# Optimization experiments

Hardware: AMD Instinct MI355X
Metric: run time of the kernel (lower is better)

Reference implementation:

```python
import jax, jax.numpy as jnp
import numpy as np

# graph sizes
G, P, EP = 128, 256, 1024          # graphs, nodes/graph, edges/graph
N, E = G * P, G * EP
C, KENS, S = 4, 2, 1               # centroids, ensembles, samples
R = S * KENS                       # repeats
F, DE, D, OUT = 64, 16, 128, 10


def setup_inputs() -> dict:
    key = jax.random.key(0)
    ks = jax.random.split(key, 24)
    off = (jnp.arange(G, dtype=jnp.int32) * P)[:, None]
    src = (jax.random.randint(ks[0], (G, EP), 0, P, dtype=jnp.int32) + off).reshape(-1)
    dst = (jax.random.randint(ks[1], (G, EP), 0, P, dtype=jnp.int32) + off).reshape(-1)
    edge_index = jnp.stack([src, dst])            # [2, E], edges stay within graphs
    batch = jnp.repeat(jnp.arange(G, dtype=jnp.int32), P)  # [N]
    rn = lambda k, shp, s: jax.random.normal(k, shp, jnp.float32) * s
    return {
        "x_feat": rn(ks[2], (N, F), 1.0),
        "edge_attr": rn(ks[3], (E, DE), 1.0),
        "W_atom": rn(ks[4], (F, D), 0.1), "b_atom": jnp.zeros((D,), jnp.float32),
        "W_score": rn(ks[5], (D, C * KENS), 0.1),
        "W_edge": rn(ks[6], (DE, D), 0.1),
        "W_b2c": rn(ks[7], (D, D), 0.1),
        "W_bb": rn(ks[8], (D, D), 0.1), "W_bc": rn(ks[9], (D, D), 0.1),
        "W_cb": rn(ks[10], (D, D), 0.1), "W_cc": rn(ks[11], (D, D), 0.1),
        "W_sb": rn(ks[12], (D, D), 0.1), "W_sc": rn(ks[13], (D, D), 0.1),
        "W_inter": rn(ks[14], (D, D), 0.1), "b_inter": jnp.zeros((D,), jnp.float32),
        "W_out": rn(ks[15], (D, OUT), 0.1), "b_out": jnp.zeros((OUT,), jnp.float32),
        "edge_index": edge_index, "batch": batch,
    }


def reference(x_feat, edge_attr, W_atom, b_atom, W_score, W_edge, W_b2c,
              W_bb, W_bc, W_cb, W_cc, W_sb, W_sc, W_inter, b_inter,
              W_out, b_out, edge_index, batch):
    src, dst = edge_index[0], edge_index[1]
    # atom encoder + scorer + softmax sampler (marginals)
    x = x_feat @ W_atom + b_atom                                  # [N,D]
    scores = (x @ W_score).reshape(N, C, KENS)
    marg = jax.nn.softmax(scores, axis=1)                         # over centroids
    nm = jnp.broadcast_to(marg[None], (S, N, C, KENS))            # [S,N,C,KENS]
    nm = jnp.transpose(nm, (0, 3, 2, 1)).reshape(R, C, N)         # [R,C,N]
    em = nm[:, :, src] * nm[:, :, dst]                            # edge_mask [R,C,E]
    # base2centroid: masked MP on base graph + weighted segment-mean pooling
    edge_emb = edge_attr @ W_edge                                 # [E,D]
    h = jax.nn.relu(x @ W_b2c)                                    # [N,D]
    m = h[src] + edge_emb                                         # [E,D]
    agg = jnp.zeros((R, C, N, D), m.dtype).at[:, :, dst].add(em[..., None] * m)
    hm = h[None, None] + agg                                      # [R,C,N,D]
    denom = jnp.zeros((R, C, G), nm.dtype).at[:, :, batch].add(nm)
    num = jnp.zeros((R, C, G, D), hm.dtype).at[:, :, batch].add(nm[..., None] * hm)
    cent_x = jnp.transpose(num / (denom[..., None] + 1e-6), (0, 2, 1, 3))  # [R,G,C,D]
    # intra centroid-pair edge weights: triu pairs + diag, scatter over graphs
    iu, ju = np.triu_indices(C, 1)
    pi = np.concatenate([iu, np.arange(C)])
    pj = np.concatenate([ju, np.arange(C)])
    e2g = batch[src]
    w = jnp.zeros((R, pi.size, G), nm.dtype).at[:, :, e2g].add(
        nm[:, pi][:, :, src] * nm[:, pj][:, :, dst])              # [R,10,G]
    w = w.at[:, -C:, :].multiply(0.5)                             # halve diagonal counts
    wt = jnp.transpose(w, (0, 2, 1))                              # [R,G,10]
    Wcc = jnp.zeros((R, G, C, C), nm.dtype)
    Wcc = Wcc.at[:, :, pi, pj].add(wt).at[:, :, pj, pi].add(wt)   # to_undirected
    dg = jnp.arange(C)
    Wcc = Wcc.at[:, :, dg, dg].multiply(0.5)                      # self loops counted once
    Wcc = Wcc / (jax.lax.stop_gradient(jnp.max(Wcc)) + 1e-9)      # detached-max norm
    # hetero GNN layer: base->base, base->centroid, centroid->centroid, centroid->base
    agg_bb = jnp.zeros((N, D), x.dtype).at[dst].add(x[src] + edge_emb)           # [N,D]
    agg_bc = jnp.transpose(
        jnp.zeros((R, C, G, D), x.dtype).at[:, :, batch].add(nm[..., None] * x[None, None]),
        (0, 2, 1, 3))                                             # [R,G,C,D]
    agg_cc = jnp.einsum('rgij,rgjd->rgid', Wcc, cent_x)
    h_cent = jax.nn.relu(agg_bc @ W_bc + agg_cc @ W_cc + cent_x @ W_sc)          # [R,G,C,D]
    agg_cb = jnp.einsum('rcn,rncd->rnd', nm, h_cent[:, batch])                   # [R,N,D]
    h_base = jax.nn.relu(agg_bb[None] @ W_bb + agg_cb @ W_cb + x[None] @ W_sb)   # [R,N,D]
    # inter-ensemble mean pool, inter head, intra mean graph pool, intra head
    node_emb = jnp.mean(h_base, axis=0) @ W_inter + b_inter                      # [N,D]
    graph_emb = jnp.zeros((G, D), node_emb.dtype).at[batch].add(node_emb) / P    # [G,D]
    return graph_emb @ W_out + b_out                                             # [G,OUT]
```

## Files before the change

kernel.cpp:

```cpp
#include <hip/hip_runtime.h>
#include <hip/hip_bf16.h>

#define Nn 32768
#define Ee 131072
#define Gg 128
#define Dd 128

using bf16 = __hip_bfloat16;
typedef __attribute__((ext_vector_type(8))) short bf16x8;
typedef __attribute__((ext_vector_type(4))) float f32x4;

__device__ __forceinline__ float b2f(bf16 v){ return __bfloat162float(v); }
__device__ __forceinline__ bf16  f2b(float v){ return __float2bfloat16(v); }
__device__ __forceinline__ unsigned short bf16bits(float v){
  union { bf16 b; unsigned short u; } cv; cv.b = f2b(v); return cv.u;
}
__device__ __forceinline__ unsigned int packxh(float xv, float hv){
  return ((unsigned int)bf16bits(hv) << 16) | (unsigned int)bf16bits(xv);
}
__device__ __forceinline__ float upk_x(unsigned int v){ return __uint_as_float(v << 16); }
__device__ __forceinline__ float upk_h(unsigned int v){ return __uint_as_float(v & 0xffff0000u); }

__global__ __launch_bounds__(128)
void k_wrep(const float* __restrict__ Wbb, const float* __restrict__ Wsb,
            const float* __restrict__ Wcb, unsigned short* __restrict__ Wbbp,
            unsigned short* __restrict__ Wsbp, unsigned short* __restrict__ Wcbp) {
  int mat = blockIdx.x >> 7, n = blockIdx.x & 127, k = threadIdx.x;
  const float* src = (mat == 0) ? Wbb : (mat == 1) ? Wsb : Wcb;
  unsigned short* dst = (mat == 0) ? Wbbp : (mat == 1) ? Wsbp : Wcbp;
  dst[n*128 + k] = bf16bits(src[k*128 + n]);
}

__global__ __launch_bounds__(256)
void k_atom(const float* __restrict__ xf, const float* __restrict__ Wa,
            const float* __restrict__ ba, const float* __restrict__ Wsc,
            const float* __restrict__ Wb2c,
            unsigned int* __restrict__ xh, float* __restrict__ nmt) {
  __shared__ float sxf[32*64];
  __shared__ float sx[32*128];
  __shared__ float ss[32*8];
  int tid = threadIdx.x, n0 = blockIdx.x * 32;
  int ct = tid & 31, rt = tid >> 5;
  int c0 = ct*4, r0 = rt*4;
  for (int j = tid; j < 2048; j += 256) sxf[j] = xf[n0*64 + j];
  __syncthreads();
  float acc[4][4];
  #pragma unroll
  for (int i = 0; i < 4; ++i)
    #pragma unroll
    for (int j = 0; j < 4; ++j) acc[i][j] = ba[c0+j];
  for (int k = 0; k < 64; ++k) {
    float4 bv = *reinterpret_cast<const float4*>(&Wa[k*128 + c0]);
    #pragma unroll
    for (int i = 0; i < 4; ++i) {
      float a = sxf[(r0+i)*64 + k];
      acc[i][0] += a*bv.x; acc[i][1] += a*bv.y; acc[i][2] += a*bv.z; acc[i][3] += a*bv.w;
    }
  }
  #pragma unroll
  for (int i = 0; i < 4; ++i)
    #pragma unroll
    for (int j = 0; j < 4; ++j) sx[(r0+i)*128 + c0+j] = acc[i][j];
  __syncthreads();
  {
    int node = tid >> 3, col = tid & 7;
    float s = 0.f;
    for (int d = 0; d < 128; ++d) s += sx[node*128 + d] * Wsc[d*8 + col];
    ss[node*8 + col] = s;
  }
  __syncthreads();
  if (tid < 64) {
    int node = tid >> 1, k = tid & 1;
    float v0 = ss[node*8 + 0 + k], v1 = ss[node*8 + 2 + k];
    float v2 = ss[node*8 + 4 + k], v3 = ss[node*8 + 6 + k];
    float mx = fmaxf(fmaxf(v0, v1), fmaxf(v2, v3));
    float e0 = expf(v0-mx), e1 = expf(v1-mx), e2 = expf(v2-mx), e3 = expf(v3-mx);
    float inv = 1.f / (e0+e1+e2+e3);
    size_t nb = (size_t)(n0 + node)*8 + k*4;
    nmt[nb+0] = e0*inv; nmt[nb+1] = e1*inv; nmt[nb+2] = e2*inv; nmt[nb+3] = e3*inv;
  }
  float acc2[4][4];
  #pragma unroll
  for (int i = 0; i < 4; ++i)
    #pragma unroll
    for (int j = 0; j < 4; ++j) acc2[i][j] = 0.f;
  for (int k = 0; k < 128; ++k) {
    float4 bv = *reinterpret_cast<const float4*>(&Wb2c[k*128 + c0]);
    #pragma unroll
    for (int i = 0; i < 4; ++i) {
      float a = sx[(r0+i)*128 + k];
      acc2[i][0] += a*bv.x; acc2[i][1] += a*bv.y; acc2[i][2] += a*bv.z; acc2[i][3] += a*bv.w;
    }
  }
  #pragma unroll
  for (int i = 0; i < 4; ++i)
    #pragma unroll
    for (int j = 0; j < 4; ++j)
      xh[(size_t)(n0+r0+i)*128 + c0+j] = packxh(acc[i][j], fmaxf(acc2[i][j], 0.f));
}

__global__ __launch_bounds__(256)
void k_csr(const int* __restrict__ ei, const float* __restrict__ nmt,
           int* __restrict__ order, int* __restrict__ osrc,
           int* __restrict__ rowstart, float* __restrict__ den) {
  __shared__ int cnt[256], off[256], sdl[1024];
  __shared__ float sden[256*8];
  int t = threadIdx.x, g = blockIdx.x;
  cnt[t] = 0;
  __syncthreads();
  #pragma unroll
  for (int j = 0; j < 4; ++j) {
    int e = t + j*256;
    int dl = ei[Ee + g*1024 + e] - g*256;
    sdl[e] = dl;
    atomicAdd(&cnt[dl], 1);
  }
  {
    const float4* p = reinterpret_cast<const float4*>(nmt + (size_t)(g*256 + t)*8);
    float4 a = p[0], b = p[1];
    sden[t*8+0]=a.x; sden[t*8+1]=a.y; sden[t*8+2]=a.z; sden[t*8+3]=a.w;
    sden[t*8+4]=b.x; sden[t*8+5]=b.y; sden[t*8+6]=b.z; sden[t*8+7]=b.w;
  }
  __syncthreads();
  off[t] = cnt[t];
  __syncthreads();
  for (int s = 1; s < 256; s <<= 1) {
    int v = (t >= s) ? off[t - s] : 0;
    __syncthreads();
    off[t] += v;
    __syncthreads();
  }
  int startv = off[t] - cnt[t];
  rowstart[g*256 + t] = startv;
  off[t] = startv;
  __syncthreads();
  #pragma unroll
  for (int j = 0; j < 4; ++j) {
    int e = t + j*256;
    int pos = atomicAdd(&off[sdl[e]], 1);
    order[g*1024 + pos] = e;
    osrc[g*1024 + pos]  = ei[g*1024 + e];
  }
  if (t < 8) {
    float s = 0.f;
    for (int p = 0; p < 256; ++p) s += sden[p*8 + t];
    den[t*Gg + g] = s;
  }
}

__global__ __launch_bounds__(256)
void k_gather(const unsigned int* __restrict__ xh, const float* __restrict__ nmt,
              const float* __restrict__ ea, const float* __restrict__ We,
              const int* __restrict__ order, const int* __restrict__ osrc,
              const int* __restrict__ rowstart,
              unsigned short* __restrict__ aggbb16, float* __restrict__ pnum,
              float* __restrict__ pabc) {
  __shared__ float combN[8*128], combA[8*128];
  int t = threadIdx.x, d = t & 127, q = t >> 7;
  int g = blockIdx.x >> 4, e16 = blockIdx.x & 15;
  int nbase = g*256 + e16*16;
  float w[16];
  #pragma unroll
  for (int j = 0; j < 16; ++j) w[j] = We[j*128 + d];
  float aH[8] = {0,0,0,0,0,0,0,0};
  float aX[8] = {0,0,0,0,0,0,0,0};
  float aE[8] = {0,0,0,0,0,0,0,0};
  for (int nn = q; nn < 16; nn += 2) {
    int n = nbase + nn;
    unsigned int vn = xh[(size_t)n*128 + d];
    float xn = upk_x(vn), hn = upk_h(vn);
    const float4* pp = reinterpret_cast<const float4*>(nmt + (size_t)n*8);
    float4 p0 = pp[0], p1 = pp[1];
    float pc[8] = {p0.x,p0.y,p0.z,p0.w,p1.x,p1.y,p1.z,p1.w};
    float bsq[8];
    #pragma unroll
    for (int rc = 0; rc < 8; ++rc) {
      aH[rc] += pc[rc]*hn; aX[rc] += pc[rc]*xn;
      bsq[rc] = pc[rc]*pc[rc];
    }
    int ln = n - g*256;
    int start = rowstart[n];
    int end = (ln == 255) ? 1024 : rowstart[n+1];
    float agga = 0.f;
    for (int jj = start; jj < end; ++jj) {
      int e  = order[g*1024 + jj];
      int sg = osrc[g*1024 + jj];
      const float4* er = reinterpret_cast<const float4*>(ea + ((size_t)g*1024 + e)*16);
      float4 a0 = er[0], a1 = er[1], a2 = er[2], a3 = er[3];
      float ev = a0.x*w[0] + a0.y*w[1] + a0.z*w[2] + a0.w*w[3]
               + a1.x*w[4] + a1.y*w[5] + a1.z*w[6] + a1.w*w[7]
               + a2.x*w[8] + a2.y*w[9] + a2.z*w[10]+ a2.w*w[11]
               + a3.x*w[12]+ a3.y*w[13]+ a3.z*w[14]+ a3.w*w[15];
      unsigned int vs = xh[(size_t)sg*128 + d];
      agga += upk_x(vs) + ev;
      float hv = upk_h(vs) + ev;
      const float4* qq = reinterpret_cast<const float4*>(nmt + (size_t)sg*8);
      float4 q0 = qq[0], q1 = qq[1];
      float qc[8] = {q0.x,q0.y,q0.z,q0.w,q1.x,q1.y,q1.z,q1.w};
      #pragma unroll
      for (int rc = 0; rc < 8; ++rc) aE[rc] += bsq[rc]*qc[rc]*hv;
    }
    aggbb16[(size_t)n*128 + d] = bf16bits(agga);
  }
  if (q == 1) {
    #pragma unroll
    for (int rc = 0; rc < 8; ++rc) { combN[rc*128+d] = aH[rc]+aE[rc]; combA[rc*128+d] = aX[rc]; }
  }
  __syncthreads();
  if (q == 0) {
    #pragma unroll
    for (int rc = 0; rc < 8; ++rc) {
      pnum[(((size_t)rc*Gg + g)*16 + e16)*128 + d] = aH[rc] + aE[rc] + combN[rc*128+d];
      pabc[(((size_t)rc*Gg + g)*16 + e16)*128 + d] = aX[rc] + combA[rc*128+d];
    }
  }
}

__global__ __launch_bounds__(256)
void k_wcc(const float* __restrict__ nmt, const int* __restrict__ ei,
           float* __restrict__ wcc, unsigned int* __restrict__ maxbits) {
  __shared__ float red[20];
  int t = threadIdx.x, g = blockIdx.x;
  if (t < 20) red[t] = 0.f;
  __syncthreads();
  float w[20];
  #pragma unroll
  for (int i = 0; i < 20; ++i) w[i] = 0.f;
  #pragma unroll
  for (int j = 0; j < 4; ++j) {
    int e = g*1024 + t + j*256;
    int s = ei[e], dd = ei[Ee + e];
    const float4* ps4 = reinterpret_cast<const float4*>(nmt + (size_t)s*8);
    const float4* pt4 = reinterpret_cast<const float4*>(nmt + (size_t)dd*8);
    float4 s0 = ps4[0], s1 = ps4[1], t0 = pt4[0], t1 = pt4[1];
    float ps[8] = {s0.x,s0.y,s0.z,s0.w,s1.x,s1.y,s1.z,s1.w};
    float pt[8] = {t0.x,t0.y,t0.z,t0.w,t1.x,t1.y,t1.z,t1.w};
    #pragma unroll
    for (int r = 0; r < 2; ++r) {
      int b = r*4;
      w[r*10+0] += ps[b+0]*pt[b+1]; w[r*10+1] += ps[b+0]*pt[b+2]; w[r*10+2] += ps[b+0]*pt[b+3];
      w[r*10+3] += ps[b+1]*pt[b+2]; w[r*10+4] += ps[b+1]*pt[b+3]; w[r*10+5] += ps[b+2]*pt[b+3];
      w[r*10+6] += ps[b+0]*pt[b+0]; w[r*10+7] += ps[b+1]*pt[b+1];
      w[r*10+8] += ps[b+2]*pt[b+2]; w[r*10+9] += ps[b+3]*pt[b+3];
    }
  }
  #pragma unroll
  for (int i = 0; i < 20; ++i) {
    for (int off = 32; off > 0; off >>= 1) w[i] += __shfl_down(w[i], off);
  }
  if ((t & 63) == 0) {
    #pragma unroll
    for (int i = 0; i < 20; ++i) atomicAdd(&red[i], w[i]);
  }
  __syncthreads();
  if (t < 32) {
    int r = t >> 4, ij = t & 15, i = ij >> 2, j = ij & 3;
    float v;
    if (i == j) v = 0.5f * red[r*10 + 6 + i];
    else { int a = i < j ? i : j, b = i < j ? j : i;
           int p = (a == 0) ? (b - 1) : (a == 1) ? (b + 1) : 5;
           v = red[r*10 + p]; }
    wcc[(r*Gg + g)*16 + ij] = v;
    atomicMax(maxbits, __float_as_uint(v));
  }
}

__global__ __launch_bounds__(128)
void k_hcent(const float* __restrict__ pnum, const float* __restrict__ den,
             const float* __restrict__ pabc, const float* __restrict__ wcc,
             const unsigned int* __restrict__ maxbits,
             const float* __restrict__ Wbc, const float* __restrict__ Wcc_,
             const float* __restrict__ Wsc2, float* __restrict__ hcent) {
  __shared__ float scent[512], sbc[512], sccs[512], swcc[16];
  int tid = threadIdx.x, r = blockIdx.x >> 7, g = blockIdx.x & 127;
  float inv = 1.f / (__uint_as_float(*maxbits) + 1e-9f);
  if (tid < 16) swcc[tid] = wcc[(r*Gg + g)*16 + tid] * inv;
  for (int c = 0; c < 4; ++c) {
    int rc = r*4 + c;
    float nv = 0.f, av = 0.f;
    #pragma unroll
    for (int s = 0; s < 16; ++s) {
      nv += pnum[(((size_t)rc*Gg + g)*16 + s)*128 + tid];
      av += pabc[(((size_t)rc*Gg + g)*16 + s)*128 + tid];
    }
    float dn = den[rc*Gg + g] + 1e-6f;
    scent[c*128 + tid] = nv / dn;
    sbc[c*128 + tid]   = av;
  }
  __syncthreads();
  for (int i = 0; i < 4; ++i) {
    sccs[i*128 + tid] = swcc[i*4+0]*scent[tid]       + swcc[i*4+1]*scent[128 + tid]
                      + swcc[i*4+2]*scent[256 + tid] + swcc[i*4+3]*scent[384 + tid];
  }
  __syncthreads();
  for (int c = 0; c < 4; ++c) {
    float acc = 0.f;
    for (int k = 0; k < 128; ++k) {
      acc += sbc[c*128 + k]   * Wbc[k*128 + tid];
      acc += sccs[c*128 + k]  * Wcc_[k*128 + tid];
      acc += scent[c*128 + k] * Wsc2[k*128 + tid];
    }
    hcent[((r*Gg + g)*4 + c)*128 + tid] = fmaxf(acc, 0.f);
  }
}

__global__ __launch_bounds__(256)
void k_hbase(const unsigned short* __restrict__ aggbb16,
             const unsigned int* __restrict__ xh,
             const float* __restrict__ nmt, const float* __restrict__ hcent,
             const unsigned short* __restrict__ Wbbp,
             const unsigned short* __restrict__ Wsbp,
             const unsigned short* __restrict__ Wcbp,
             float* __restrict__ gsum) {
  __shared__ unsigned short A1[64*136];
  __shared__ unsigned short A2[64*136];
  __shared__ float shc[512];
  __shared__ float snm[256];
  __shared__ float pred[128];
  int tid = threadIdx.x, n0 = blockIdx.x*64, g = n0 >> 8;
  int lane = tid & 63, wv = tid >> 6;
  int m = lane & 15, quad = lane >> 4;
  int rbase = wv*16;
  for (int j = tid; j < 1024; j += 256) {
    int row = j >> 4, col = (j & 15) * 8;
    uint4 v = *reinterpret_cast<const uint4*>(aggbb16 + (size_t)(n0+row)*128 + col);
    *reinterpret_cast<uint4*>(&A1[row*136 + col]) = v;
  }
  for (int j = tid; j < 2048; j += 256) {
    int row = j >> 5, col = (j & 31) * 4;
    uint4 v = *reinterpret_cast<const uint4*>(xh + (size_t)(n0+row)*128 + col);
    uint2 o;
    o.x = (v.x & 0xffffu) | (v.y << 16);
    o.y = (v.z & 0xffffu) | (v.w << 16);
    *reinterpret_cast<uint2*>(&A2[row*136 + col]) = o;
  }
  __syncthreads();
  f32x4 bb[8];
  #pragma unroll
  for (int nt = 0; nt < 8; ++nt) bb[nt] = (f32x4){0.f,0.f,0.f,0.f};
  const short* a1r = (const short*)&A1[(rbase + m)*136];
  const short* a2r = (const short*)&A2[(rbase + m)*136];
  #pragma unroll
  for (int nt = 0; nt < 8; ++nt) {
    #pragma unroll
    for (int kk = 0; kk < 4; ++kk) {
      int ko = kk*32 + quad*8;
      bf16x8 av1 = *reinterpret_cast<const bf16x8*>(a1r + ko);
      bf16x8 wv1 = *reinterpret_cast<const bf16x8*>((const short*)Wbbp + (nt*16 + m)*128 + ko);
      bb[nt] = __builtin_amdgcn_mfma_f32_16x16x32_bf16(av1, wv1, bb[nt], 0, 0, 0);
      bf16x8 av2 = *reinterpret_cast<const bf16x8*>(a2r + ko);
      bf16x8 wv2 = *reinterpret_cast<const bf16x8*>((const short*)Wsbp + (nt*16 + m)*128 + ko);
      bb[nt] = __builtin_amdgcn_mfma_f32_16x16x32_bf16(av2, wv2, bb[nt], 0, 0, 0);
    }
  }
  __syncthreads();
  unsigned short* SB = A2;
  f32x4 msum[8];
  #pragma unroll
  for (int nt = 0; nt < 8; ++nt) msum[nt] = (f32x4){0.f,0.f,0.f,0.f};
  for (int r = 0; r < 2; ++r) {
    for (int j = tid; j < 512; j += 256) shc[j] = hcent[((size_t)(r*Gg + g)*4)*128 + j];
    if (tid < 256) snm[tid] = nmt[(size_t)(n0 + (tid >> 2))*8 + r*4 + (tid & 3)];
    __syncthreads();
    for (int j = tid; j < 8192; j += 256) {
      int node = j >> 7, k = j & 127;
      float v = snm[node*4+0]*shc[k]       + snm[node*4+1]*shc[128 + k]
              + snm[node*4+2]*shc[256 + k] + snm[node*4+3]*shc[384 + k];
      SB[node*136 + k] = bf16bits(v);
    }
    __syncthreads();
    f32x4 aw[8];
    #pragma unroll
    for (int nt = 0; nt < 8; ++nt) aw[nt] = (f32x4){0.f,0.f,0.f,0.f};
    const short* sbr = (const short*)&SB[(rbase + m)*136];
    #pragma unroll
    for (int nt = 0; nt < 8; ++nt) {
      #pragma unroll
      for (int kk = 0; kk < 4; ++kk) {
        int ko = kk*32 + quad*8;
        bf16x8 av = *reinterpret_cast<const bf16x8*>(sbr + ko);
        bf16x8 wvv = *reinterpret_cast<const bf16x8*>((const short*)Wcbp + (nt*16 + m)*128 + ko);
        aw[nt] = __builtin_amdgcn_mfma_f32_16x16x32_bf16(av, wvv, aw[nt], 0, 0, 0);
      }
    }
    #pragma unroll
    for (int nt = 0; nt < 8; ++nt) {
      #pragma unroll
      for (int i = 0; i < 4; ++i)
        msum[nt][i] += 0.5f * fmaxf(bb[nt][i] + aw[nt][i], 0.f);
    }
    __syncthreads();
  }
  if (tid < 128) pred[tid] = 0.f;
  __syncthreads();
  #pragma unroll
  for (int nt = 0; nt < 8; ++nt) {
    float s = msum[nt][0] + msum[nt][1] + msum[nt][2] + msum[nt][3];
    atomicAdd(&pred[nt*16 + m], s);
  }
  __syncthreads();
  if (tid < 128) atomicAdd(&gsum[g*128 + tid], pred[tid]);
}

__global__ __launch_bounds__(128)
void k_out(const float* __restrict__ gsum, const float* __restrict__ Wint,
           const float* __restrict__ bint, const float* __restrict__ Wout,
           const float* __restrict__ bout, float* __restrict__ out) {
  __shared__ float ss[128], sge[128];
  int tid = threadIdx.x, g = blockIdx.x;
  ss[tid] = gsum[g*128 + tid] * (1.f/256.f);
  __syncthreads();
  float ge = bint[tid];
  for (int k = 0; k < 128; ++k) ge += ss[k] * Wint[k*128 + tid];
  sge[tid] = ge;
  __syncthreads();
  if (tid < 10) {
    float o = bout[tid];
    for (int d = 0; d < 128; ++d) o += sge[d] * Wout[d*10 + tid];
    out[g*10 + tid] = o;
  }
}

extern "C" void kernel_launch(void* const* d_in, const int* in_sizes, int n_in,
                              void* d_out, int out_size, void* d_ws, size_t ws_size,
                              hipStream_t stream) {
  const float* xf   = (const float*)d_in[0];
  const float* ea   = (const float*)d_in[1];
  const float* Wa   = (const float*)d_in[2];
  const float* ba   = (const float*)d_in[3];
  const float* Wsc  = (const float*)d_in[4];
  const float* We   = (const float*)d_in[5];
  const float* Wb2c = (const float*)d_in[6];
  const float* Wbb  = (const float*)d_in[7];
  const float* Wbc  = (const float*)d_in[8];
  const float* Wcb  = (const float*)d_in[9];
  const float* WccW = (const float*)d_in[10];
  const float* Wsb  = (const float*)d_in[11];
  const float* Wsc2 = (const float*)d_in[12];
  const float* Wint = (const float*)d_in[13];
  const float* bint = (const float*)d_in[14];
  const float* Wout = (const float*)d_in[15];
  const float* bout = (const float*)d_in[16];
  const int*   ei   = (const int*)d_in[17];

  float* ws    = (float*)d_ws;
  unsigned int* xh = (unsigned int*)ws;
  float* nmt   = ws + 4194304;
  float* hcent = ws + 4456448;
  float* wcc   = ws + 4587520;
  unsigned short* aggbb16 = (unsigned short*)(ws + 4591616);
  int*   order = (int*)(ws + 6688768);
  int*   osrc  = (int*)(ws + 6819840);
  int*   rowst = (int*)(ws + 6950912);
  float* pnum  = ws + 6983680;
  float* pabc  = ws + 9080832;
  float* den   = ws + 11177984;
  float* gsum  = ws + 11179008;
  unsigned int* maxbits = (unsigned int*)(ws + 11195392);
  unsigned short* Wbbp = (unsigned short*)(ws + 11195456);
  unsigned short* Wsbp = (unsigned short*)(ws + 11203648);
  unsigned short* Wcbp = (unsigned short*)(ws + 11211840);

  hipMemsetAsync(gsum, 0, (16384 + 64) * sizeof(float), stream);

  k_wrep  <<<3*128, 128, 0, stream>>>(Wbb, Wsb, Wcb, Wbbp, Wsbp, Wcbp);
  k_atom  <<<Nn/32, 256, 0, stream>>>(xf, Wa, ba, Wsc, Wb2c, xh, nmt);
  k_csr   <<<Gg,    256, 0, stream>>>(ei, nmt, order, osrc, rowst, den);
  k_gather<<<Gg*16, 256, 0, stream>>>(xh, nmt, ea, We, order, osrc, rowst,
                                      aggbb16, pnum, pabc);
  k_wcc   <<<Gg,    256, 0, stream>>>(nmt, ei, wcc, maxbits);
  k_hcent <<<2*Gg,  128, 0, stream>>>(pnum, den, pabc, wcc, maxbits, Wbc, WccW, Wsc2, hcent);
  k_hbase <<<Nn/64, 256, 0, stream>>>(aggbb16, xh, nmt, hcent, Wbbp, Wsbp, Wcbp, gsum);
  k_out   <<<Gg,    128, 0, stream>>>(gsum, Wint, bint, Wout, bout, (float*)d_out);
}
```

Measured before the change: 307.3 us.

## Factor edge-embedding projection out of gather via per-node and per-graph edge-attr sums

Edge-attribute projection through W_edge is moved out of the per-edge, per-feature inner loop. The CSR kernel now precomputes per-destination sums of edge attributes, and a new edge-scatter kernel precomputes per-source centroid weights (beta) and per-graph weighted edge-attr sums, which are applied later through W_edge in the centroid kernel. The gather inner loop shrinks to a single source-feature load per edge, which removes the redundant 16-wide dot product repeated across 128 feature lanes. It also includes smaller tweaks: staging W_score in shared memory and register-blocking the centroid matmul over 4 centroids. The cost is extra serial loops over edges in the per-graph kernels and more workspace traffic.

```diff
diff --git a/kernel.cpp b/kernel.cpp
--- a/kernel.cpp
+++ b/kernel.cpp
@@ -5,6 +5,7 @@
 #define Ee 131072
 #define Gg 128
 #define Dd 128
+#define ASTR 1032
 
 using bf16 = __hip_bfloat16;
 typedef __attribute__((ext_vector_type(8))) short bf16x8;
@@ -39,10 +40,12 @@
   __shared__ float sxf[32*64];
   __shared__ float sx[32*128];
   __shared__ float ss[32*8];
+  __shared__ float sWsc[1024];
   int tid = threadIdx.x, n0 = blockIdx.x * 32;
   int ct = tid & 31, rt = tid >> 5;
   int c0 = ct*4, r0 = rt*4;
   for (int j = tid; j < 2048; j += 256) sxf[j] = xf[n0*64 + j];
+  for (int j = tid; j < 1024; j += 256) sWsc[j] = Wsc[j];
   __syncthreads();
   float acc[4][4];
   #pragma unroll
@@ -65,7 +68,7 @@
   {
     int node = tid >> 3, col = tid & 7;
     float s = 0.f;
-    for (int d = 0; d < 128; ++d) s += sx[node*128 + d] * Wsc[d*8 + col];
+    for (int d = 0; d < 128; ++d) s += sx[node*128 + d] * sWsc[d*8 + col];
     ss[node*8 + col] = s;
   }
   __syncthreads();
@@ -101,9 +104,10 @@
 
 __global__ __launch_bounds__(256)
 void k_csr(const int* __restrict__ ei, const float* __restrict__ nmt,
-           int* __restrict__ order, int* __restrict__ osrc,
-           int* __restrict__ rowstart, float* __restrict__ den) {
-  __shared__ int cnt[256], off[256], sdl[1024];
+           const float* __restrict__ ea,
+           int* __restrict__ osrc, int* __restrict__ rowstart,
+           float* __restrict__ sea, float* __restrict__ den) {
+  __shared__ int cnt[256], off[256], sdl[1024], sorder[1024];
   __shared__ float sden[256*8];
   int t = threadIdx.x, g = blockIdx.x;
   cnt[t] = 0;
@@ -131,6 +135,7 @@
     __syncthreads();
   }
   int startv = off[t] - cnt[t];
+  int mycnt = cnt[t];
   rowstart[g*256 + t] = startv;
   off[t] = startv;
   __syncthreads();
@@ -138,9 +143,26 @@
   for (int j = 0; j < 4; ++j) {
     int e = t + j*256;
     int pos = atomicAdd(&off[sdl[e]], 1);
-    order[g*1024 + pos] = e;
-    osrc[g*1024 + pos]  = ei[g*1024 + e];
-  }
+    sorder[pos] = e;
+    osrc[g*1024 + pos] = ei[g*1024 + e];
+  }
+  __syncthreads();
+  float s0x=0,s0y=0,s0z=0,s0w=0, s1x=0,s1y=0,s1z=0,s1w=0;
+  float s2x=0,s2y=0,s2z=0,s2w=0, s3x=0,s3y=0,s3z=0,s3w=0;
+  for (int jj = startv; jj < startv + mycnt; ++jj) {
+    int e = sorder[jj];
+    const float4* er = reinterpret_cast<const float4*>(ea + ((size_t)g*1024 + e)*16);
+    float4 a0 = er[0], a1 = er[1], a2 = er[2], a3 = er[3];
+    s0x+=a0.x; s0y+=a0.y; s0z+=a0.z; s0w+=a0.w;
+    s1x+=a1.x; s1y+=a1.y; s1z+=a1.z; s1w+=a1.w;
+    s2x+=a2.x; s2y+=a2.y; s2z+=a2.z; s2w+=a2.w;
+    s3x+=a3.x; s3y+=a3.y; s3z+=a3.z; s3w+=a3.w;
+  }
+  float4* so = reinterpret_cast<float4*>(sea + (size_t)(g*256 + t)*16);
+  so[0] = make_float4(s0x,s0y,s0z,s0w);
+  so[1] = make_float4(s1x,s1y,s1z,s1w);
+  so[2] = make_float4(s2x,s2y,s2z,s2w);
+  so[3] = make_float4(s3x,s3y,s3z,s3w);
   if (t < 8) {
     float s = 0.f;
     for (int p = 0; p < 256; ++p) s += sden[p*8 + t];
@@ -149,78 +171,16 @@
 }
 
 __global__ __launch_bounds__(256)
-void k_gather(const unsigned int* __restrict__ xh, const float* __restrict__ nmt,
-              const float* __restrict__ ea, const float* __restrict__ We,
-              const int* __restrict__ order, const int* __restrict__ osrc,
-              const int* __restrict__ rowstart,
-              unsigned short* __restrict__ aggbb16, float* __restrict__ pnum,
-              float* __restrict__ pabc) {
-  __shared__ float combN[8*128], combA[8*128];
-  int t = threadIdx.x, d = t & 127, q = t >> 7;
-  int g = blockIdx.x >> 4, e16 = blockIdx.x & 15;
-  int nbase = g*256 + e16*16;
-  float w[16];
-  #pragma unroll
-  for (int j = 0; j < 16; ++j) w[j] = We[j*128 + d];
-  float aH[8] = {0,0,0,0,0,0,0,0};
-  float aX[8] = {0,0,0,0,0,0,0,0};
-  float aE[8] = {0,0,0,0,0,0,0,0};
-  for (int nn = q; nn < 16; nn += 2) {
-    int n = nbase + nn;
-    unsigned int vn = xh[(size_t)n*128 + d];
-    float xn = upk_x(vn), hn = upk_h(vn);
-    const float4* pp = reinterpret_cast<const float4*>(nmt + (size_t)n*8);
-    float4 p0 = pp[0], p1 = pp[1];
-    float pc[8] = {p0.x,p0.y,p0.z,p0.w,p1.x,p1.y,p1.z,p1.w};
-    float bsq[8];
-    #pragma unroll
-    for (int rc = 0; rc < 8; ++rc) {
-      aH[rc] += pc[rc]*hn; aX[rc] += pc[rc]*xn;
-      bsq[rc] = pc[rc]*pc[rc];
-    }
-    int ln = n - g*256;
-    int start = rowstart[n];
-    int end = (ln == 255) ? 1024 : rowstart[n+1];
-    float agga = 0.f;
-    for (int jj = start; jj < end; ++jj) {
-      int e  = order[g*1024 + jj];
-      int sg = osrc[g*1024 + jj];
-      const float4* er = reinterpret_cast<const float4*>(ea + ((size_t)g*1024 + e)*16);
-      float4 a0 = er[0], a1 = er[1], a2 = er[2], a3 = er[3];
-      float ev = a0.x*w[0] + a0.y*w[1] + a0.z*w[2] + a0.w*w[3]
-               + a1.x*w[4] + a1.y*w[5] + a1.z*w[6] + a1.w*w[7]
-               + a2.x*w[8] + a2.y*w[9] + a2.z*w[10]+ a2.w*w[11]
-               + a3.x*w[12]+ a3.y*w[13]+ a3.z*w[14]+ a3.w*w[15];
-      unsigned int vs = xh[(size_t)sg*128 + d];
-      agga += upk_x(vs) + ev;
-      float hv = upk_h(vs) + ev;
-      const float4* qq = reinterpret_cast<const float4*>(nmt + (size_t)sg*8);
-      float4 q0 = qq[0], q1 = qq[1];
-      float qc[8] = {q0.x,q0.y,q0.z,q0.w,q1.x,q1.y,q1.z,q1.w};
-      #pragma unroll
-      for (int rc = 0; rc < 8; ++rc) aE[rc] += bsq[rc]*qc[rc]*hv;
-    }
-    aggbb16[(size_t)n*128 + d] = bf16bits(agga);
-  }
-  if (q == 1) {
-    #pragma unroll
-    for (int rc = 0; rc < 8; ++rc) { combN[rc*128+d] = aH[rc]+aE[rc]; combA[rc*128+d] = aX[rc]; }
-  }
-  __syncthreads();
-  if (q == 0) {
-    #pragma unroll
-    for (int rc = 0; rc < 8; ++rc) {
-      pnum[(((size_t)rc*Gg + g)*16 + e16)*128 + d] = aH[rc] + aE[rc] + combN[rc*128+d];
-      pabc[(((size_t)rc*Gg + g)*16 + e16)*128 + d] = aX[rc] + combA[rc*128+d];
-    }
-  }
-}
-
-__global__ __launch_bounds__(256)
-void k_wcc(const float* __restrict__ nmt, const int* __restrict__ ei,
-           float* __restrict__ wcc, unsigned int* __restrict__ maxbits) {
+void k_edgesc(const int* __restrict__ ei, const float* __restrict__ nmt,
+              const float* __restrict__ ea, float* __restrict__ wcc,
+              unsigned int* __restrict__ maxbits, float* __restrict__ bnm,
+              float* __restrict__ gea) {
+  __shared__ float salpha[8*ASTR];
+  __shared__ float sbeta[8*256];
   __shared__ float red[20];
+  __shared__ float geap[4*128];
   int t = threadIdx.x, g = blockIdx.x;
+  for (int j = t; j < 2048; j += 256) sbeta[j] = 0.f;
   if (t < 20) red[t] = 0.f;
   __syncthreads();
   float w[20];
@@ -228,13 +188,13 @@
   for (int i = 0; i < 20; ++i) w[i] = 0.f;
   #pragma unroll
   for (int j = 0; j < 4; ++j) {
-    int e = g*1024 + t + j*256;
-    int s = ei[e], dd = ei[Ee + e];
+    int e = t + j*256;
+    int s = ei[g*1024 + e], dd = ei[Ee + g*1024 + e];
     const float4* ps4 = reinterpret_cast<const float4*>(nmt + (size_t)s*8);
     const float4* pt4 = reinterpret_cast<const float4*>(nmt + (size_t)dd*8);
-    float4 s0 = ps4[0], s1 = ps4[1], t0 = pt4[0], t1 = pt4[1];
-    float ps[8] = {s0.x,s0.y,s0.z,s0.w,s1.x,s1.y,s1.z,s1.w};
-    float pt[8] = {t0.x,t0.y,t0.z,t0.w,t1.x,t1.y,t1.z,t1.w};
+    float4 sv0 = ps4[0], sv1 = ps4[1], tv0 = pt4[0], tv1 = pt4[1];
+    float ps[8] = {sv0.x,sv0.y,sv0.z,sv0.w,sv1.x,sv1.y,sv1.z,sv1.w};
+    float pt[8] = {tv0.x,tv0.y,tv0.z,tv0.w,tv1.x,tv1.y,tv1.z,tv1.w};
     #pragma unroll
     for (int r = 0; r < 2; ++r) {
       int b = r*4;
@@ -243,10 +203,17 @@
       w[r*10+6] += ps[b+0]*pt[b+0]; w[r*10+7] += ps[b+1]*pt[b+1];
       w[r*10+8] += ps[b+2]*pt[b+2]; w[r*10+9] += ps[b+3]*pt[b+3];
     }
+    int sl = s - g*256;
+    #pragma unroll
+    for (int rc = 0; rc < 8; ++rc) {
+      float al = ps[rc]*pt[rc]*pt[rc];
+      salpha[rc*ASTR + e] = al;
+      atomicAdd(&sbeta[rc*256 + sl], al);
+    }
   }
   #pragma unroll
   for (int i = 0; i < 20; ++i) {
-    for (int off = 32; off > 0; off >>= 1) w[i] += __shfl_down(w[i], off);
+    for (int off2 = 32; off2 > 0; off2 >>= 1) w[i] += __shfl_down(w[i], off2);
   }
   if ((t & 63) == 0) {
     #pragma unroll
@@ -263,11 +230,96 @@
     wcc[(r*Gg + g)*16 + ij] = v;
     atomicMax(maxbits, __float_as_uint(v));
   }
+  int wv = t >> 6, l = t & 63;
+  int j16 = l & 15, rb = l >> 4;
+  float acc0 = 0.f, acc1 = 0.f;
+  int ebase = wv*256;
+  for (int ee = 0; ee < 256; ++ee) {
+    float eav = ea[((size_t)g*1024 + ebase + ee)*16 + j16];
+    acc0 += salpha[rb*ASTR + ebase + ee] * eav;
+    acc1 += salpha[(rb+4)*ASTR + ebase + ee] * eav;
+  }
+  geap[wv*128 + l]      = acc0;
+  geap[wv*128 + 64 + l] = acc1;
+  __syncthreads();
+  if (t < 128) {
+    float s = geap[t] + geap[128+t] + geap[256+t] + geap[384+t];
+    int rc = t >> 4, j = t & 15;
+    gea[((size_t)rc*Gg + g)*16 + j] = s;
+  }
+  {
+    float b0 = sbeta[0*256+t], b1 = sbeta[1*256+t], b2 = sbeta[2*256+t], b3 = sbeta[3*256+t];
+    float b4 = sbeta[4*256+t], b5 = sbeta[5*256+t], b6 = sbeta[6*256+t], b7 = sbeta[7*256+t];
+    float4* bo = reinterpret_cast<float4*>(bnm + (size_t)(g*256 + t)*8);
+    bo[0] = make_float4(b0,b1,b2,b3);
+    bo[1] = make_float4(b4,b5,b6,b7);
+  }
+}
+
+__global__ __launch_bounds__(256)
+void k_gather(const unsigned int* __restrict__ xh, const float* __restrict__ nmt,
+              const float* __restrict__ bnm, const float* __restrict__ sea,
+              const float* __restrict__ We, const int* __restrict__ osrc,
+              const int* __restrict__ rowstart,
+              unsigned short* __restrict__ aggbb16, float* __restrict__ pnum,
+              float* __restrict__ pabc) {
+  __shared__ float combN[8*128], combA[8*128];
+  int t = threadIdx.x, d = t & 127, q = t >> 7;
+  int g = blockIdx.x >> 4, e16 = blockIdx.x & 15;
+  int nbase = g*256 + e16*16;
+  float w[16];
+  #pragma unroll
+  for (int j = 0; j < 16; ++j) w[j] = We[j*128 + d];
+  float aH[8] = {0,0,0,0,0,0,0,0};
+  float aX[8] = {0,0,0,0,0,0,0,0};
+  for (int nn = q; nn < 16; nn += 2) {
+    int n = nbase + nn;
+    unsigned int vn = xh[(size_t)n*128 + d];
+    float xn = upk_x(vn), hn = upk_h(vn);
+    const float4* pp = reinterpret_cast<const float4*>(nmt + (size_t)n*8);
+    float4 p0 = pp[0], p1 = pp[1];
+    float pc[8] = {p0.x,p0.y,p0.z,p0.w,p1.x,p1.y,p1.z,p1.w};
+    const float4* bp = reinterpret_cast<const float4*>(bnm + (size_t)n*8);
+    float4 b0 = bp[0], b1 = bp[1];
+    float bt[8] = {b0.x,b0.y,b0.z,b0.w,b1.x,b1.y,b1.z,b1.w};
+    #pragma unroll
+    for (int rc = 0; rc < 8; ++rc) {
+      aH[rc] += (pc[rc] + bt[rc])*hn;
+      aX[rc] += pc[rc]*xn;
+    }
+    const float4* sp = reinterpret_cast<const float4*>(sea + (size_t)n*16);
+    float4 s0 = sp[0], s1 = sp[1], s2 = sp[2], s3 = sp[3];
+    float agg = s0.x*w[0] + s0.y*w[1] + s0.z*w[2] + s0.w*w[3]
+              + s1.x*w[4] + s1.y*w[5] + s1.z*w[6] + s1.w*w[7]
+              + s2.x*w[8] + s2.y*w[9] + s2.z*w[10]+ s2.w*w[11]
+              + s3.x*w[12]+ s3.y*w[13]+ s3.z*w[14]+ s3.w*w[15];
+    int ln = n - g*256;
+    int start = rowstart[n];
+    int end = (ln == 255) ? 1024 : rowstart[n+1];
+    for (int jj = start; jj < end; ++jj) {
+      int sg = osrc[g*1024 + jj];
+      agg += upk_x(xh[(size_t)sg*128 + d]);
+    }
+    aggbb16[(size_t)n*128 + d] = bf16bits(agg);
+  }
+  if (q == 1) {
+    #pragma unroll
+    for (int rc = 0; rc < 8; ++rc) { combN[rc*128+d] = aH[rc]; combA[rc*128+d] = aX[rc]; }
+  }
+  __syncthreads();
+  if (q == 0) {
+    #pragma unroll
+    for (int rc = 0; rc < 8; ++rc) {
+      pnum[(((size_t)rc*Gg + g)*16 + e16)*128 + d] = aH[rc] + combN[rc*128+d];
+      pabc[(((size_t)rc*Gg + g)*16 + e16)*128 + d] = aX[rc] + combA[rc*128+d];
+    }
+  }
 }
 
 __global__ __launch_bounds__(128)
 void k_hcent(const float* __restrict__ pnum, const float* __restrict__ den,
-             const float* __restrict__ pabc, const float* __restrict__ wcc,
+             const float* __restrict__ pabc, const float* __restrict__ gea,
+             const float* __restrict__ We, const float* __restrict__ wcc,
              const unsigned int* __restrict__ maxbits,
              const float* __restrict__ Wbc, const float* __restrict__ Wcc_,
              const float* __restrict__ Wsc2, float* __restrict__ hcent) {
@@ -283,6 +335,9 @@
       nv += pnum[(((size_t)rc*Gg + g)*16 + s)*128 + tid];
       av += pabc[(((size_t)rc*Gg + g)*16 + s)*128 + tid];
     }
+    const float* geag = gea + ((size_t)rc*Gg + g)*16;
+    #pragma unroll
+    for (int j = 0; j < 16; ++j) nv += geag[j] * We[j*128 + tid];
     float dn = den[rc*Gg + g] + 1e-6f;
     scent[c*128 + tid] = nv / dn;
     sbc[c*128 + tid]   = av;
@@ -293,15 +348,16 @@
                       + swcc[i*4+2]*scent[256 + tid] + swcc[i*4+3]*scent[384 + tid];
   }
   __syncthreads();
-  for (int c = 0; c < 4; ++c) {
-    float acc = 0.f;
-    for (int k = 0; k < 128; ++k) {
-      acc += sbc[c*128 + k]   * Wbc[k*128 + tid];
-      acc += sccs[c*128 + k]  * Wcc_[k*128 + tid];
-      acc += scent[c*128 + k] * Wsc2[k*128 + tid];
-    }
-    hcent[((r*Gg + g)*4 + c)*128 + tid] = fmaxf(acc, 0.f);
-  }
+  float acc[4] = {0.f, 0.f, 0.f, 0.f};
+  for (int k = 0; k < 128; ++k) {
+    float wb = Wbc[k*128 + tid], wc = Wcc_[k*128 + tid], ws2 = Wsc2[k*128 + tid];
+    #pragma unroll
+    for (int c = 0; c < 4; ++c)
+      acc[c] += sbc[c*128 + k]*wb + sccs[c*128 + k]*wc + scent[c*128 + k]*ws2;
+  }
+  #pragma unroll
+  for (int c = 0; c < 4; ++c)
+    hcent[((r*Gg + g)*4 + c)*128 + tid] = fmaxf(acc[c], 0.f);
 }
 
 __global__ __launch_bounds__(256)
@@ -449,27 +505,30 @@
   float* hcent = ws + 4456448;
   float* wcc   = ws + 4587520;
   unsigned short* aggbb16 = (unsigned short*)(ws + 4591616);
-  int*   order = (int*)(ws + 6688768);
-  int*   osrc  = (int*)(ws + 6819840);
-  int*   rowst = (int*)(ws + 6950912);
-  float* pnum  = ws + 6983680;
-  float* pabc  = ws + 9080832;
-  float* den   = ws + 11177984;
-  float* gsum  = ws + 11179008;
-  unsigned int* maxbits = (unsigned int*)(ws + 11195392);
-  unsigned short* Wbbp = (unsigned short*)(ws + 11195456);
-  unsigned short* Wsbp = (unsigned short*)(ws + 11203648);
-  unsigned short* Wcbp = (unsigned short*)(ws + 11211840);
+  int*   osrc  = (int*)(ws + 6688768);
+  int*   rowst = (int*)(ws + 6819840);
+  float* sea   = ws + 6852608;
+  float* bnm   = ws + 7376896;
+  float* gea   = ws + 7639040;
+  float* pnum  = ws + 7655424;
+  float* pabc  = ws + 9752576;
+  float* den   = ws + 11849728;
+  float* gsum  = ws + 11850752;
+  unsigned int* maxbits = (unsigned int*)(ws + 11867136);
+  unsigned short* Wbbp = (unsigned short*)(ws + 11867200);
+  unsigned short* Wsbp = (unsigned short*)(ws + 11875392);
+  unsigned short* Wcbp = (unsigned short*)(ws + 11883584);
 
   hipMemsetAsync(gsum, 0, (16384 + 64) * sizeof(float), stream);
 
   k_wrep  <<<3*128, 128, 0, stream>>>(Wbb, Wsb, Wcb, Wbbp, Wsbp, Wcbp);
   k_atom  <<<Nn/32, 256, 0, stream>>>(xf, Wa, ba, Wsc, Wb2c, xh, nmt);
-  k_csr   <<<Gg,    256, 0, stream>>>(ei, nmt, order, osrc, rowst, den);
-  k_gather<<<Gg*16, 256, 0, stream>>>(xh, nmt, ea, We, order, osrc, rowst,
+  k_csr   <<<Gg,    256, 0, stream>>>(ei, nmt, ea, osrc, rowst, sea, den);
+  k_edgesc<<<Gg,    256, 0, stream>>>(ei, nmt, ea, wcc, maxbits, bnm, gea);
+  k_gather<<<Gg*16, 256, 0, stream>>>(xh, nmt, bnm, sea, We, osrc, rowst,
                                       aggbb16, pnum, pabc);
-  k_wcc   <<<Gg,    256, 0, stream>>>(nmt, ei, wcc, maxbits);
-  k_hcent <<<2*Gg,  128, 0, stream>>>(pnum, den, pabc, wcc, maxbits, Wbc, WccW, Wsc2, hcent);
+  k_hcent <<<2*Gg,  128, 0, stream>>>(pnum, den, pabc, gea, We, wcc, maxbits,
+                                      Wbc, WccW, Wsc2, hcent);
   k_hbase <<<Nn/64, 256, 0, stream>>>(aggbb16, xh, nmt, hcent, Wbbp, Wsbp, Wcbp, gsum);
   k_out   <<<Gg,    128, 0, stream>>>(gsum, Wint, bint, Wout, bout, (float*)d_out);
 }
```

Measured after the change: 293.3 us. 1.05x faster.
